# Kernel tuning notes

Hardware: AMD Instinct MI355X
Metric: run time of the kernel (lower is better)

## Reference

```python
import jax, jax.numpy as jnp
import numpy as np

B, N, D, H, DH, E, BIAS_DIM = 8, 512, 512, 8, 64, 32768, 8

def setup_inputs() -> dict:
    key = jax.random.key(0)
    ks = jax.random.split(key, 10)
    states = jax.random.normal(ks[0], (B, N, D), jnp.float32)
    key_states = jax.random.normal(ks[1], (B, N, D), jnp.float32)
    # causal mask, broadcastable over heads: [B,1,N,N]
    masks = jnp.broadcast_to(jnp.tril(jnp.ones((N, N), jnp.float32)), (B, 1, N, N))
    edge_type = jax.random.randint(ks[2], (E, 1), 0, BIAS_DIM, jnp.int32)
    b_idx = jax.random.randint(ks[3], (E, 1), 0, B, jnp.int32)
    q_idx = jax.random.randint(ks[4], (E, 1), 0, N, jnp.int32)
    k_idx = jax.random.randint(ks[5], (E, 1), 0, N, jnp.int32)
    attention_bias = jnp.concatenate([edge_type, b_idx, q_idx, k_idx], axis=1)
    s = 0.05
    Wq = jax.random.normal(ks[6], (D, H, DH), jnp.float32) * s
    Wk = jax.random.normal(ks[7], (D, H, DH), jnp.float32) * s
    Wv = jax.random.normal(ks[8], (D, H, DH), jnp.float32) * s
    k2 = jax.random.split(ks[9], 3)
    Wo = jax.random.normal(k2[0], (H, DH, D), jnp.float32) * s
    bias_embs = jax.random.normal(k2[1], (BIAS_DIM, DH), jnp.float32) * s
    bias_scalar = jax.random.normal(k2[2], (DH, 1), jnp.float32) * s
    return {"states": states, "key_states": key_states, "masks": masks,
            "attention_bias": attention_bias, "Wq": Wq, "Wk": Wk, "Wv": Wv,
            "Wo": Wo, "bias_embs": bias_embs, "bias_scalar": bias_scalar}

def reference(states, key_states, masks, attention_bias, Wq, Wk, Wv, Wo, bias_embs, bias_scalar):
    q = jnp.einsum('btd,dha->btha', states, Wq)
    k = jnp.einsum('btd,dha->btha', key_states, Wk)
    v = jnp.einsum('btd,dha->btha', key_states, Wv)
    alpha = jnp.einsum('bkha,bqha->bhqk', k, q)  # [B,H,Q,K]
    # sparse edge bias: embed edge types, project to scalar, scatter into [B,Q,K]
    et = attention_bias[:, 0]
    bias_vals = (bias_embs[et] @ bias_scalar)[:, 0]  # [E]
    bq, bk = alpha.shape[2], alpha.shape[3]
    bias_mat = jnp.zeros((alpha.shape[0], bq, bk), alpha.dtype)
    bias_mat = bias_mat.at[attention_bias[:, 1], attention_bias[:, 2], attention_bias[:, 3]].add(bias_vals)
    summed_keys = jnp.sum(k, axis=-1)  # [B,K,H]
    alpha = alpha + jnp.einsum('bqk,bkh->bhqk', bias_mat, summed_keys)
    alpha = alpha * jax.lax.rsqrt(jnp.float32(DH))
    neg = jnp.finfo(jnp.float32).min
    alpha = alpha * masks + (1.0 - jnp.ceil(masks)) * neg
    alpha = jax.nn.softmax(alpha, axis=-1)
    alpha = alpha * masks
    context = jnp.einsum('bhqk,bkha->bqha', alpha, v)
    return jnp.einsum('btha,had->btd', context, Wo)
```

## Files before the change

### kernel.cpp

```cpp
#include <hip/hip_runtime.h>

typedef unsigned short u16;
typedef unsigned int u32;
typedef __bf16 bf16x8 __attribute__((ext_vector_type(8)));
typedef float f32x4 __attribute__((ext_vector_type(4)));
typedef u16 u16x8 __attribute__((ext_vector_type(8)));
typedef u16 u16x4 __attribute__((ext_vector_type(4)));


__device__ __forceinline__ u16 f2b(float f) {
  union { float f; u32 i; } v; v.f = f;
  u32 r = v.i + 0x7fffu + ((v.i >> 16) & 1u);
  return (u16)(r >> 16);
}
__device__ __forceinline__ float b2f(u16 u) {
  union { u32 i; float f; } v; v.i = ((u32)u) << 16; return v.f;
}

__global__ __launch_bounds__(256) void prologue(
    const float* __restrict__ states, const float* __restrict__ key_states,
    const float* __restrict__ Wq, const float* __restrict__ Wk,
    const float* __restrict__ Wv, const float* __restrict__ Wo,
    const int* __restrict__ ab, const float* __restrict__ be,
    const float* __restrict__ bsc,
    u16* __restrict__ sb, u16* __restrict__ kbin, u16* __restrict__ wbase,
    float* __restrict__ bias_mat, int n_edges) {
  __shared__ u16 t[32][33];
  __shared__ float tv[8];
  int bid = blockIdx.x;
  int tid = threadIdx.x;
  if (bid < 2048) {
    const float* src = (bid >= 1024) ? key_states : states;
    u16* dst = (bid >= 1024) ? kbin : sb;
    int gid = (bid & 1023) * 256 + tid;
    const float4* sp = (const float4*)src + (size_t)gid * 2;
    float4 x0 = sp[0], x1 = sp[1];
    u16x8 p;
    p[0] = f2b(x0.x); p[1] = f2b(x0.y); p[2] = f2b(x0.z); p[3] = f2b(x0.w);
    p[4] = f2b(x1.x); p[5] = f2b(x1.y); p[6] = f2b(x1.z); p[7] = f2b(x1.w);
    *(u16x8*)(dst + (size_t)gid * 8) = p;
  } else if (bid < 3072) {
    int tt = bid - 2048;
    int z = tt >> 8, rem = tt & 255;
    int bx = rem & 15, by = rem >> 4;
    const float* src; float sc = 1.f;
    if (z == 0)      { src = Wq; sc = 0.125f; }
    else if (z == 1) { src = Wk; }
    else if (z == 2) { src = Wv; }
    else             { src = Wo; }
    u16* dst = wbase + (size_t)z * 262144;
    int tx = tid & 31, ty = tid >> 5;
    int c0 = bx * 32, r0 = by * 32;
    #pragma unroll
    for (int i = ty; i < 32; i += 8) t[i][tx] = f2b(src[(r0 + i) * 512 + c0 + tx] * sc);
    __syncthreads();
    #pragma unroll
    for (int i = ty; i < 32; i += 8) dst[(c0 + i) * 512 + r0 + tx] = t[tx][i];
  } else {
    if (tid < 8) {
      float s = 0.f;
      #pragma unroll
      for (int a = 0; a < 64; a++) s += be[tid * 64 + a] * bsc[a];
      tv[tid] = s * 0.125f;
    }
    __syncthreads();
    int e = (bid - 3072) * 256 + tid;
    if (e < n_edges) {
      int et = ab[e * 4 + 0];
      int b  = ab[e * 4 + 1];
      int qi = ab[e * 4 + 2];
      int ki = ab[e * 4 + 3];
      atomicAdd(&bias_mat[((size_t)b * 512 + qi) * 512 + ki], tv[et]);
    }
  }
}

__global__ __launch_bounds__(256) void qkv_gemm(const u16* __restrict__ sb,
                                                const u16* __restrict__ kbin,
                                                const u16* __restrict__ wT,
                                                u16* __restrict__ qb,
                                                u16* __restrict__ kbo,
                                                u16* __restrict__ vtb,
                                                float* __restrict__ summed) {
  __shared__ u16 As[64 * 72];
  __shared__ u16 Bs[128 * 72];
  __shared__ float ssum[4][64];
  int tid = threadIdx.x;
  int lane = tid & 63, wave = tid >> 6;
  int quad = lane >> 4, ln = lane & 15;
  int row0 = blockIdx.x * 64;
  int col0 = blockIdx.y * 128;
  const u16* A = (col0 < 512) ? sb : kbin;
  int ara = tid >> 2, aca = (tid & 3) * 16;
  int arb = tid >> 1, acb = (tid & 1) * 32;

  f32x4 acc[4][2];
  #pragma unroll
  for (int i = 0; i < 4; i++)
    #pragma unroll
    for (int j = 0; j < 2; j++) acc[i][j] = (f32x4){0.f, 0.f, 0.f, 0.f};

  const u16* ap = A + (size_t)(row0 + ara) * 512 + aca;
  const u16* bp = wT + (size_t)(col0 + arb) * 512 + acb;

  u16x8 ra0, ra1, rb0, rb1, rb2, rb3;
  ra0 = *(const u16x8*)(ap + 0);  ra1 = *(const u16x8*)(ap + 8);
  rb0 = *(const u16x8*)(bp + 0);  rb1 = *(const u16x8*)(bp + 8);
  rb2 = *(const u16x8*)(bp + 16); rb3 = *(const u16x8*)(bp + 24);

  for (int k0 = 0; k0 < 512; k0 += 64) {
    __syncthreads();
    *(u16x8*)&As[ara * 72 + aca + 0] = ra0;  *(u16x8*)&As[ara * 72 + aca + 8] = ra1;
    *(u16x8*)&Bs[arb * 72 + acb + 0]  = rb0;  *(u16x8*)&Bs[arb * 72 + acb + 8]  = rb1;
    *(u16x8*)&Bs[arb * 72 + acb + 16] = rb2;  *(u16x8*)&Bs[arb * 72 + acb + 24] = rb3;
    __syncthreads();
    if (k0 < 448) {
      int kn = k0 + 64;
      ra0 = *(const u16x8*)(ap + kn + 0);  ra1 = *(const u16x8*)(ap + kn + 8);
      rb0 = *(const u16x8*)(bp + kn + 0);  rb1 = *(const u16x8*)(bp + kn + 8);
      rb2 = *(const u16x8*)(bp + kn + 16); rb3 = *(const u16x8*)(bp + kn + 24);
    }
    #pragma unroll
    for (int s = 0; s < 2; s++) {
      bf16x8 af[4], bfv[2];
      #pragma unroll
      for (int i = 0; i < 4; i++)
        af[i] = *(bf16x8*)&As[(i * 16 + ln) * 72 + s * 32 + quad * 8];
      #pragma unroll
      for (int j = 0; j < 2; j++)
        bfv[j] = *(bf16x8*)&Bs[(wave * 32 + j * 16 + ln) * 72 + s * 32 + quad * 8];
      #pragma unroll
      for (int i = 0; i < 4; i++)
        #pragma unroll
        for (int j = 0; j < 2; j++)
          acc[i][j] = __builtin_amdgcn_mfma_f32_16x16x32_bf16(af[i], bfv[j], acc[i][j], 0, 0, 0);
    }
  }

  int region = col0 >> 9;
  int nbase = col0 & 511;
  if (region <= 1) {
    u16* Cout = region ? kbo : qb;
    #pragma unroll
    for (int i = 0; i < 4; i++)
      #pragma unroll
      for (int j = 0; j < 2; j++) {
        int mb = row0 + i * 16 + quad * 4;
        int n = nbase + wave * 32 + j * 16 + ln;
        #pragma unroll
        for (int r = 0; r < 4; r++)
          Cout[(size_t)(mb + r) * 512 + n] = f2b(acc[i][j][r]);
      }
    if (region == 1) {
      #pragma unroll
      for (int i = 0; i < 4; i++)
        #pragma unroll
        for (int r = 0; r < 4; r++) {
          float v = acc[i][0][r] + acc[i][1][r];
          v += __shfl_xor(v, 1);
          v += __shfl_xor(v, 2);
          v += __shfl_xor(v, 4);
          v += __shfl_xor(v, 8);
          if (ln == 0) ssum[wave][i * 16 + quad * 4 + r] = v;
        }
      __syncthreads();
      if (tid < 128) {
        int hl = tid >> 6, row = tid & 63;
        float s = ssum[hl * 2][row] + ssum[hl * 2 + 1][row];
        int m = row0 + row;
        int b = m >> 9, t = m & 511;
        int h = (nbase >> 6) + hl;
        summed[((size_t)(b * 8 + h)) * 512 + t] = s;
      }
    }
  } else {
    #pragma unroll
    for (int i = 0; i < 4; i++)
      #pragma unroll
      for (int j = 0; j < 2; j++) {
        int mb = row0 + i * 16 + quad * 4;
        int bb = mb >> 9, t0 = mb & 511;
        int a_abs = nbase + wave * 32 + j * 16 + ln;
        int h = a_abs >> 6, a = a_abs & 63;
        u16x4 p;
        p[0] = f2b(acc[i][j][0]); p[1] = f2b(acc[i][j][1]);
        p[2] = f2b(acc[i][j][2]); p[3] = f2b(acc[i][j][3]);
        *(u16x4*)&vtb[(((size_t)bb * 8 + h) * 64 + a) * 512 + t0] = p;
      }
  }
}

__global__ __launch_bounds__(256) void out_gemm(const u16* __restrict__ A,
                                                const u16* __restrict__ BT,
                                                float* __restrict__ C) {
  __shared__ u16 As[64 * 72];
  __shared__ u16 Bs[64 * 72];
  int tid = threadIdx.x;
  int lane = tid & 63, wave = tid >> 6;
  int quad = lane >> 4, ln = lane & 15;
  int wr = wave >> 1, wc = wave & 1;
  int row0 = blockIdx.x * 64;
  int col0 = blockIdx.y * 64;
  int ar = tid >> 2, ac = (tid & 3) * 16;

  f32x4 acc[2][2];
  #pragma unroll
  for (int i = 0; i < 2; i++)
    #pragma unroll
    for (int j = 0; j < 2; j++) acc[i][j] = (f32x4){0.f, 0.f, 0.f, 0.f};

  const u16* ap = A + (size_t)(row0 + ar) * 512 + ac;
  const u16* bp = BT + (size_t)(col0 + ar) * 512 + ac;

  u16x8 ra0, ra1, rb0, rb1;
  ra0 = *(const u16x8*)(ap + 0); ra1 = *(const u16x8*)(ap + 8);
  rb0 = *(const u16x8*)(bp + 0); rb1 = *(const u16x8*)(bp + 8);

  for (int k0 = 0; k0 < 512; k0 += 64) {
    __syncthreads();
    *(u16x8*)&As[ar * 72 + ac + 0] = ra0;  *(u16x8*)&As[ar * 72 + ac + 8] = ra1;
    *(u16x8*)&Bs[ar * 72 + ac + 0] = rb0;  *(u16x8*)&Bs[ar * 72 + ac + 8] = rb1;
    __syncthreads();
    if (k0 < 448) {
      int kn = k0 + 64;
      ra0 = *(const u16x8*)(ap + kn + 0); ra1 = *(const u16x8*)(ap + kn + 8);
      rb0 = *(const u16x8*)(bp + kn + 0); rb1 = *(const u16x8*)(bp + kn + 8);
    }
    #pragma unroll
    for (int s = 0; s < 2; s++) {
      bf16x8 af[2], bfv[2];
      #pragma unroll
      for (int i = 0; i < 2; i++)
        af[i] = *(bf16x8*)&As[(wr * 32 + i * 16 + ln) * 72 + s * 32 + quad * 8];
      #pragma unroll
      for (int j = 0; j < 2; j++)
        bfv[j] = *(bf16x8*)&Bs[(wc * 32 + j * 16 + ln) * 72 + s * 32 + quad * 8];
      #pragma unroll
      for (int i = 0; i < 2; i++)
        #pragma unroll
        for (int j = 0; j < 2; j++)
          acc[i][j] = __builtin_amdgcn_mfma_f32_16x16x32_bf16(af[i], bfv[j], acc[i][j], 0, 0, 0);
    }
  }
  #pragma unroll
  for (int i = 0; i < 2; i++)
    #pragma unroll
    for (int j = 0; j < 2; j++) {
      int mb = row0 + wr * 32 + i * 16 + quad * 4;
      int n = col0 + wc * 32 + j * 16 + ln;
      #pragma unroll
      for (int r = 0; r < 4; r++)
        C[(size_t)(mb + r) * 512 + n] = acc[i][j][r];
    }
}

__global__ __launch_bounds__(256) void attn_mfma(const u16* __restrict__ q,
                                                 const u16* __restrict__ k,
                                                 const u16* __restrict__ vt,
                                                 const float* __restrict__ bias_mat,
                                                 const float* __restrict__ summed,
                                                 u16* __restrict__ ctx,
                                                 float* __restrict__ Opart,
                                                 float* __restrict__ ml) {
  __shared__ u16 Qs[64 * 72];
  __shared__ u16 Ks[64 * 72];
  __shared__ u16 Vt[64 * 72];
  __shared__ u16 Ps[4][16 * 72];
  int tid = threadIdx.x;
  int wave = tid >> 6, lane = tid & 63;
  int quad = lane >> 4, ln = lane & 15;
  int p2 = blockIdx.x;
  int bh, u;
  {
    const int fours[6] = {3, 4, 6, 8, 10, 11};
    const int threes[2] = {2, 9};
    const int ones[2] = {0, 5};
    const int twos[2] = {1, 7};
    if (p2 < 384)      { bh = p2 & 63; u = fours[p2 >> 6]; }
    else if (p2 < 512) { int q2 = p2 - 384; bh = q2 & 63; u = threes[q2 >> 6]; }
    else if (p2 < 640) { int q2 = p2 - 512; bh = q2 & 63; u = ones[q2 >> 6]; }
    else               { int q2 = p2 - 640; bh = q2 & 63; u = twos[q2 >> 6]; }
  }
  int b = bh >> 3, h = bh & 7;
  int qt, kb0, kbe, part = 0;
  bool partial;
  if (u < 4) { qt = u; kb0 = 0; kbe = u; partial = false; }
  else {
    int v = u - 4; qt = 4 + (v >> 1); part = v & 1; partial = true;
    if (part == 0) { kb0 = 0; kbe = 3; } else { kb0 = 4; kbe = qt; }
  }
  int q0 = qt * 64;

  int sr = tid >> 2;
  int sc2 = (tid & 3) * 16;

  {
    const u16* qp = q + ((size_t)(b * 512 + q0 + sr)) * 512 + h * 64 + sc2;
    *(u16x8*)&Qs[sr * 72 + sc2] = *(const u16x8*)qp;
    *(u16x8*)&Qs[sr * 72 + sc2 + 8] = *(const u16x8*)(qp + 8);
  }

  float m_r[4], l_r[4];
  f32x4 o[4];
  #pragma unroll
  for (int r = 0; r < 4; r++) { m_r[r] = -3.40282347e38f; l_r[r] = 0.f; }
  #pragma unroll
  for (int nt = 0; nt < 4; nt++) o[nt] = (f32x4){0.f, 0.f, 0.f, 0.f};

  const u16* kp0 = k + ((size_t)(b * 512 + sr)) * 512 + h * 64 + sc2;
  const u16* vp0 = vt + ((size_t)(bh * 64 + sr)) * 512 + sc2;

  u16x8 rk0 = *(const u16x8*)(kp0 + (size_t)kb0 * 64 * 512);
  u16x8 rk1 = *(const u16x8*)(kp0 + (size_t)kb0 * 64 * 512 + 8);
  u16x8 rv0 = *(const u16x8*)(vp0 + kb0 * 64);
  u16x8 rv1 = *(const u16x8*)(vp0 + kb0 * 64 + 8);

  int qrow = q0 + wave * 16 + quad * 4;

  float c_skv[4], c_bias[4][4];
  #pragma unroll
  for (int nt = 0; nt < 4; nt++) {
    int t = kb0 * 64 + nt * 16 + ln;
    c_skv[nt] = summed[bh * 512 + t];
    const float* bp2 = bias_mat + ((size_t)(b * 512 + qrow)) * 512 + t;
    #pragma unroll
    for (int r = 0; r < 4; r++) c_bias[nt][r] = bp2[(size_t)r * 512];
  }

  for (int kb = kb0; kb <= kbe; kb++) {
    __syncthreads();
    *(u16x8*)&Ks[sr * 72 + sc2] = rk0;
    *(u16x8*)&Ks[sr * 72 + sc2 + 8] = rk1;
    *(u16x8*)&Vt[sr * 72 + sc2] = rv0;
    *(u16x8*)&Vt[sr * 72 + sc2 + 8] = rv1;
    __syncthreads();

    float n_skv[4], n_bias[4][4];
    if (kb < kbe) {
      const u16* kp = kp0 + (size_t)(kb + 1) * 64 * 512;
      const u16* vp = vp0 + (kb + 1) * 64;
      rk0 = *(const u16x8*)kp;
      rk1 = *(const u16x8*)(kp + 8);
      rv0 = *(const u16x8*)vp;
      rv1 = *(const u16x8*)(vp + 8);
      #pragma unroll
      for (int nt = 0; nt < 4; nt++) {
        int t = (kb + 1) * 64 + nt * 16 + ln;
        n_skv[nt] = summed[bh * 512 + t];
        const float* bp2 = bias_mat + ((size_t)(b * 512 + qrow)) * 512 + t;
        #pragma unroll
        for (int r = 0; r < 4; r++) n_bias[nt][r] = bp2[(size_t)r * 512];
      }
    }

    bf16x8 aq0 = *(bf16x8*)&Qs[(wave * 16 + ln) * 72 + quad * 8];
    bf16x8 aq1 = *(bf16x8*)&Qs[(wave * 16 + ln) * 72 + 32 + quad * 8];
    f32x4 s[4];
    #pragma unroll
    for (int nt = 0; nt < 4; nt++) {
      bf16x8 b0 = *(bf16x8*)&Ks[(nt * 16 + ln) * 72 + quad * 8];
      bf16x8 b1 = *(bf16x8*)&Ks[(nt * 16 + ln) * 72 + 32 + quad * 8];
      s[nt] = (f32x4){0.f, 0.f, 0.f, 0.f};
      s[nt] = __builtin_amdgcn_mfma_f32_16x16x32_bf16(aq0, b0, s[nt], 0, 0, 0);
      s[nt] = __builtin_amdgcn_mfma_f32_16x16x32_bf16(aq1, b1, s[nt], 0, 0, 0);
    }

    #pragma unroll
    for (int nt = 0; nt < 4; nt++) {
      int t = kb * 64 + nt * 16 + ln;
      #pragma unroll
      for (int r = 0; r < 4; r++) {
        float val = s[nt][r] + c_bias[nt][r] * c_skv[nt];
        s[nt][r] = (t <= qrow + r) ? val : -3.40282347e38f;
      }
    }

    float alpha[4];
    #pragma unroll
    for (int r = 0; r < 4; r++) {
      float tm = fmaxf(fmaxf(s[0][r], s[1][r]), fmaxf(s[2][r], s[3][r]));
      #pragma unroll
      for (int off = 8; off; off >>= 1) tm = fmaxf(tm, __shfl_xor(tm, off));
      float mn = fmaxf(m_r[r], tm);
      alpha[r] = __expf(m_r[r] - mn);
      m_r[r] = mn;
      float rs = 0.f;
      #pragma unroll
      for (int nt = 0; nt < 4; nt++) {
        float pp = __expf(s[nt][r] - mn);
        s[nt][r] = pp;
        rs += pp;
      }
      #pragma unroll
      for (int off = 8; off; off >>= 1) rs += __shfl_xor(rs, off);
      l_r[r] = l_r[r] * alpha[r] + rs;
    }

    #pragma unroll
    for (int nt = 0; nt < 4; nt++)
      #pragma unroll
      for (int r = 0; r < 4; r++)
        Ps[wave][(quad * 4 + r) * 72 + nt * 16 + ln] = f2b(s[nt][r]);
    #pragma unroll
    for (int nt = 0; nt < 4; nt++)
      #pragma unroll
      for (int r = 0; r < 4; r++)
        o[nt][r] *= alpha[r];

    bf16x8 ap0 = *(bf16x8*)&Ps[wave][ln * 72 + quad * 8];
    bf16x8 ap1 = *(bf16x8*)&Ps[wave][ln * 72 + 32 + quad * 8];
    #pragma unroll
    for (int nt = 0; nt < 4; nt++) {
      bf16x8 b0 = *(bf16x8*)&Vt[(nt * 16 + ln) * 72 + quad * 8];
      bf16x8 b1 = *(bf16x8*)&Vt[(nt * 16 + ln) * 72 + 32 + quad * 8];
      o[nt] = __builtin_amdgcn_mfma_f32_16x16x32_bf16(ap0, b0, o[nt], 0, 0, 0);
      o[nt] = __builtin_amdgcn_mfma_f32_16x16x32_bf16(ap1, b1, o[nt], 0, 0, 0);
    }

    if (kb < kbe) {
      #pragma unroll
      for (int nt = 0; nt < 4; nt++) {
        c_skv[nt] = n_skv[nt];
        #pragma unroll
        for (int r = 0; r < 4; r++) c_bias[nt][r] = n_bias[nt][r];
      }
    }
  }

  if (!partial) {
    #pragma unroll
    for (int r = 0; r < 4; r++) {
      float inv = 1.f / l_r[r];
      int qr2 = qrow + r;
      u16* dst = ctx + ((size_t)(b * 512 + qr2)) * 512 + h * 64;
      #pragma unroll
      for (int nt = 0; nt < 4; nt++)
        dst[nt * 16 + ln] = f2b(o[nt][r] * inv);
    }
  } else {
    #pragma unroll
    for (int r = 0; r < 4; r++) {
      int row = qrow + r - 256;
      float* dst = Opart + (((size_t)(part * 64 + bh)) * 256 + row) * 64;
      #pragma unroll
      for (int nt = 0; nt < 4; nt++)
        dst[nt * 16 + ln] = o[nt][r];
    }
    if (ln == 0) {
      #pragma unroll
      for (int r = 0; r < 4; r++) {
        int row = qrow + r - 256;
        float* mp = ml + (((size_t)(part * 64 + bh)) * 256 + row) * 2;
        mp[0] = m_r[r];
        mp[1] = l_r[r];
      }
    }
  }
}

__global__ __launch_bounds__(256) void attn_merge(const float* __restrict__ Opart,
                                                  const float* __restrict__ ml,
                                                  u16* __restrict__ ctx) {
  int gid = blockIdx.x * 256 + threadIdx.x;
  int col = gid & 63;
  int row = (gid >> 6) & 255;
  int bh = gid >> 14;
  size_t i0 = (size_t)bh * 256 + row;
  size_t i1 = (size_t)(64 + bh) * 256 + row;
  float m0 = ml[i0 * 2], l0 = ml[i0 * 2 + 1];
  float m1 = ml[i1 * 2], l1 = ml[i1 * 2 + 1];
  float m = fmaxf(m0, m1);
  float a0 = __expf(m0 - m), a1 = __expf(m1 - m);
  float l = l0 * a0 + l1 * a1;
  float O0 = Opart[i0 * 64 + col], O1 = Opart[i1 * 64 + col];
  float val = (O0 * a0 + O1 * a1) / l;
  int b = bh >> 3, h = bh & 7, qrow = 256 + row;
  ctx[((size_t)(b * 512 + qrow)) * 512 + h * 64 + col] = f2b(val);
}

extern "C" void kernel_launch(void* const* d_in, const int* in_sizes, int n_in,
                              void* d_out, int out_size, void* d_ws, size_t ws_size,
                              hipStream_t stream) {
  const float* states     = (const float*)d_in[0];
  const float* key_states = (const float*)d_in[1];
  const int*   ab         = (const int*)d_in[3];
  const float* Wq         = (const float*)d_in[4];
  const float* Wk         = (const float*)d_in[5];
  const float* Wv         = (const float*)d_in[6];
  const float* Wo         = (const float*)d_in[7];
  const float* be         = (const float*)d_in[8];
  const float* bsc        = (const float*)d_in[9];
  float* out = (float*)d_out;

  char* ws = (char*)d_ws;
  const size_t MB = 1024 * 1024;
  u16* wbase    = (u16*)(ws);
  u16* wot      = (u16*)(ws + 1536 * 1024);
  u16* sb       = (u16*)(ws + 2 * MB);
  u16* kbin     = (u16*)(ws + 6 * MB);
  u16* qb       = (u16*)(ws + 10 * MB);
  u16* kbo      = (u16*)(ws + 14 * MB);
  u16* vtb      = (u16*)(ws + 18 * MB);
  u16* ctxb     = (u16*)(ws + 22 * MB);
  float* bias_m = (float*)(ws + 26 * MB);
  float* summed = (float*)(ws + 34 * MB);
  float* Opart  = (float*)(ws + 35 * MB);
  float* mlbuf  = (float*)(ws + 43 * MB);

  int n_edges = in_sizes[3] / 4;

  hipMemsetAsync(bias_m, 0, (size_t)8 * MB, stream);
  prologue<<<dim3(3072 + (n_edges + 255) / 256), 256, 0, stream>>>(
      states, key_states, Wq, Wk, Wv, Wo, ab, be, bsc, sb, kbin, wbase, bias_m, n_edges);
  qkv_gemm<<<dim3(64, 12), 256, 0, stream>>>(sb, kbin, wbase, qb, kbo, vtb, summed);
  attn_mfma<<<dim3(768), 256, 0, stream>>>(qb, kbo, vtb, bias_m, summed, ctxb, Opart, mlbuf);
  attn_merge<<<dim3(4096), 256, 0, stream>>>(Opart, mlbuf, ctxb);
  out_gemm<<<dim3(64, 8), 256, 0, stream>>>(ctxb, wot, out);
}
```

Measured before the change: 133.9 us.

## Stage GEMM and attention tiles via direct global-to-LDS loads with double buffering

Replaces the register-staged global-to-shared copies in the QKV GEMM, the output GEMM and the attention kernel with global_load_lds 16-byte transfers. These write straight into double-buffered, XOR-swizzled shared-memory tiles, and the swizzle replaces the old row padding to avoid bank conflicts. Each k-step now needs only one barrier instead of two, and the next tile's load overlaps the current tile's MFMA work. In exchange, shared memory roughly doubles for the K/V and GEMM tiles, which may lower occupancy. Correctness also depends on the async LDS writes having completed before the barrier.

```diff
diff --git a/kernel.cpp b/kernel.cpp
--- a/kernel.cpp
+++ b/kernel.cpp
@@ -15,6 +15,33 @@
 }
 __device__ __forceinline__ float b2f(u16 u) {
   union { u32 i; float f; } v; v.i = ((u32)u) << 16; return v.f;
+}
+
+#define GLL16(gp, lp)                                                      \
+  __builtin_amdgcn_global_load_lds(                                       \
+      (const __attribute__((address_space(1))) u32*)(gp),                 \
+      (__attribute__((address_space(3))) u32*)(lp), 16, 0, 0)
+
+__device__ __forceinline__ void stage64(const u16* g, u16* l, int wave, int lane) {
+  int rsub = lane >> 3;
+  int gs = (((lane & 7) ^ rsub) << 3);
+  #pragma unroll
+  for (int c = 0; c < 2; c++) {
+    int ch = wave * 2 + c;
+    GLL16(g + (size_t)(ch * 8 + rsub) * 512 + gs, l + ch * 512);
+  }
+}
+__device__ __forceinline__ void stage128(const u16* g, u16* l, int wave, int lane) {
+  int rsub = lane >> 3;
+  int gs = (((lane & 7) ^ rsub) << 3);
+  #pragma unroll
+  for (int c = 0; c < 4; c++) {
+    int ch = wave * 4 + c;
+    GLL16(g + (size_t)(ch * 8 + rsub) * 512 + gs, l + ch * 512);
+  }
+}
+__device__ __forceinline__ int swz(int row, int g) {
+  return row * 64 + ((g ^ (row & 7)) << 3);
 }
 
 __global__ __launch_bounds__(256) void prologue(
@@ -82,8 +109,8 @@
                                                 u16* __restrict__ kbo,
                                                 u16* __restrict__ vtb,
                                                 float* __restrict__ summed) {
-  __shared__ u16 As[64 * 72];
-  __shared__ u16 Bs[128 * 72];
+  __shared__ alignas(16) u16 As[2][64 * 64];
+  __shared__ alignas(16) u16 Bs[2][128 * 64];
   __shared__ float ssum[4][64];
   int tid = threadIdx.x;
   int lane = tid & 63, wave = tid >> 6;
@@ -91,8 +118,8 @@
   int row0 = blockIdx.x * 64;
   int col0 = blockIdx.y * 128;
   const u16* A = (col0 < 512) ? sb : kbin;
-  int ara = tid >> 2, aca = (tid & 3) * 16;
-  int arb = tid >> 1, acb = (tid & 1) * 32;
+  const u16* Ab = A + (size_t)row0 * 512;
+  const u16* Bb = wT + (size_t)col0 * 512;
 
   f32x4 acc[4][2];
   #pragma unroll
@@ -100,41 +127,32 @@
     #pragma unroll
     for (int j = 0; j < 2; j++) acc[i][j] = (f32x4){0.f, 0.f, 0.f, 0.f};
 
-  const u16* ap = A + (size_t)(row0 + ara) * 512 + aca;
-  const u16* bp = wT + (size_t)(col0 + arb) * 512 + acb;
-
-  u16x8 ra0, ra1, rb0, rb1, rb2, rb3;
-  ra0 = *(const u16x8*)(ap + 0);  ra1 = *(const u16x8*)(ap + 8);
-  rb0 = *(const u16x8*)(bp + 0);  rb1 = *(const u16x8*)(bp + 8);
-  rb2 = *(const u16x8*)(bp + 16); rb3 = *(const u16x8*)(bp + 24);
-
+  stage64(Ab, As[0], wave, lane);
+  stage128(Bb, Bs[0], wave, lane);
+
+  int cur = 0;
   for (int k0 = 0; k0 < 512; k0 += 64) {
     __syncthreads();
-    *(u16x8*)&As[ara * 72 + aca + 0] = ra0;  *(u16x8*)&As[ara * 72 + aca + 8] = ra1;
-    *(u16x8*)&Bs[arb * 72 + acb + 0]  = rb0;  *(u16x8*)&Bs[arb * 72 + acb + 8]  = rb1;
-    *(u16x8*)&Bs[arb * 72 + acb + 16] = rb2;  *(u16x8*)&Bs[arb * 72 + acb + 24] = rb3;
-    __syncthreads();
     if (k0 < 448) {
-      int kn = k0 + 64;
-      ra0 = *(const u16x8*)(ap + kn + 0);  ra1 = *(const u16x8*)(ap + kn + 8);
-      rb0 = *(const u16x8*)(bp + kn + 0);  rb1 = *(const u16x8*)(bp + kn + 8);
-      rb2 = *(const u16x8*)(bp + kn + 16); rb3 = *(const u16x8*)(bp + kn + 24);
+      stage64(Ab + k0 + 64, As[cur ^ 1], wave, lane);
+      stage128(Bb + k0 + 64, Bs[cur ^ 1], wave, lane);
     }
     #pragma unroll
     for (int s = 0; s < 2; s++) {
       bf16x8 af[4], bfv[2];
       #pragma unroll
       for (int i = 0; i < 4; i++)
-        af[i] = *(bf16x8*)&As[(i * 16 + ln) * 72 + s * 32 + quad * 8];
+        af[i] = *(bf16x8*)&As[cur][swz(i * 16 + ln, s * 4 + quad)];
       #pragma unroll
       for (int j = 0; j < 2; j++)
-        bfv[j] = *(bf16x8*)&Bs[(wave * 32 + j * 16 + ln) * 72 + s * 32 + quad * 8];
+        bfv[j] = *(bf16x8*)&Bs[cur][swz(wave * 32 + j * 16 + ln, s * 4 + quad)];
       #pragma unroll
       for (int i = 0; i < 4; i++)
         #pragma unroll
         for (int j = 0; j < 2; j++)
           acc[i][j] = __builtin_amdgcn_mfma_f32_16x16x32_bf16(af[i], bfv[j], acc[i][j], 0, 0, 0);
     }
+    cur ^= 1;
   }
 
   int region = col0 >> 9;
@@ -193,15 +211,16 @@
 __global__ __launch_bounds__(256) void out_gemm(const u16* __restrict__ A,
                                                 const u16* __restrict__ BT,
                                                 float* __restrict__ C) {
-  __shared__ u16 As[64 * 72];
-  __shared__ u16 Bs[64 * 72];
+  __shared__ alignas(16) u16 As[2][64 * 64];
+  __shared__ alignas(16) u16 Bs[2][64 * 64];
   int tid = threadIdx.x;
   int lane = tid & 63, wave = tid >> 6;
   int quad = lane >> 4, ln = lane & 15;
   int wr = wave >> 1, wc = wave & 1;
   int row0 = blockIdx.x * 64;
   int col0 = blockIdx.y * 64;
-  int ar = tid >> 2, ac = (tid & 3) * 16;
+  const u16* Ab = A + (size_t)row0 * 512;
+  const u16* Bb = BT + (size_t)col0 * 512;
 
   f32x4 acc[2][2];
   #pragma unroll
@@ -209,38 +228,32 @@
     #pragma unroll
     for (int j = 0; j < 2; j++) acc[i][j] = (f32x4){0.f, 0.f, 0.f, 0.f};
 
-  const u16* ap = A + (size_t)(row0 + ar) * 512 + ac;
-  const u16* bp = BT + (size_t)(col0 + ar) * 512 + ac;
-
-  u16x8 ra0, ra1, rb0, rb1;
-  ra0 = *(const u16x8*)(ap + 0); ra1 = *(const u16x8*)(ap + 8);
-  rb0 = *(const u16x8*)(bp + 0); rb1 = *(const u16x8*)(bp + 8);
-
+  stage64(Ab, As[0], wave, lane);
+  stage64(Bb, Bs[0], wave, lane);
+
+  int cur = 0;
   for (int k0 = 0; k0 < 512; k0 += 64) {
     __syncthreads();
-    *(u16x8*)&As[ar * 72 + ac + 0] = ra0;  *(u16x8*)&As[ar * 72 + ac + 8] = ra1;
-    *(u16x8*)&Bs[ar * 72 + ac + 0] = rb0;  *(u16x8*)&Bs[ar * 72 + ac + 8] = rb1;
-    __syncthreads();
     if (k0 < 448) {
-      int kn = k0 + 64;
-      ra0 = *(const u16x8*)(ap + kn + 0); ra1 = *(const u16x8*)(ap + kn + 8);
-      rb0 = *(const u16x8*)(bp + kn + 0); rb1 = *(const u16x8*)(bp + kn + 8);
+      stage64(Ab + k0 + 64, As[cur ^ 1], wave, lane);
+      stage64(Bb + k0 + 64, Bs[cur ^ 1], wave, lane);
     }
     #pragma unroll
     for (int s = 0; s < 2; s++) {
       bf16x8 af[2], bfv[2];
       #pragma unroll
       for (int i = 0; i < 2; i++)
-        af[i] = *(bf16x8*)&As[(wr * 32 + i * 16 + ln) * 72 + s * 32 + quad * 8];
+        af[i] = *(bf16x8*)&As[cur][swz(wr * 32 + i * 16 + ln, s * 4 + quad)];
       #pragma unroll
       for (int j = 0; j < 2; j++)
-        bfv[j] = *(bf16x8*)&Bs[(wc * 32 + j * 16 + ln) * 72 + s * 32 + quad * 8];
+        bfv[j] = *(bf16x8*)&Bs[cur][swz(wc * 32 + j * 16 + ln, s * 4 + quad)];
       #pragma unroll
       for (int i = 0; i < 2; i++)
         #pragma unroll
         for (int j = 0; j < 2; j++)
           acc[i][j] = __builtin_amdgcn_mfma_f32_16x16x32_bf16(af[i], bfv[j], acc[i][j], 0, 0, 0);
     }
+    cur ^= 1;
   }
   #pragma unroll
   for (int i = 0; i < 2; i++)
@@ -262,10 +275,10 @@
                                                  u16* __restrict__ ctx,
                                                  float* __restrict__ Opart,
                                                  float* __restrict__ ml) {
-  __shared__ u16 Qs[64 * 72];
-  __shared__ u16 Ks[64 * 72];
-  __shared__ u16 Vt[64 * 72];
-  __shared__ u16 Ps[4][16 * 72];
+  __shared__ alignas(16) u16 Qs[64 * 64];
+  __shared__ alignas(16) u16 Ks[2][64 * 64];
+  __shared__ alignas(16) u16 Vs[2][64 * 64];
+  __shared__ alignas(16) u16 Ps[4][16 * 72];
   int tid = threadIdx.x;
   int wave = tid >> 6, lane = tid & 63;
   int quad = lane >> 4, ln = lane & 15;
@@ -291,14 +304,13 @@
   }
   int q0 = qt * 64;
 
-  int sr = tid >> 2;
-  int sc2 = (tid & 3) * 16;
-
-  {
-    const u16* qp = q + ((size_t)(b * 512 + q0 + sr)) * 512 + h * 64 + sc2;
-    *(u16x8*)&Qs[sr * 72 + sc2] = *(const u16x8*)qp;
-    *(u16x8*)&Qs[sr * 72 + sc2 + 8] = *(const u16x8*)(qp + 8);
-  }
+  const u16* qb_ = q + ((size_t)(b * 512 + q0)) * 512 + h * 64;
+  const u16* kb_ = k + ((size_t)(b * 512)) * 512 + h * 64;
+  const u16* vb_ = vt + ((size_t)bh * 64) * 512;
+
+  stage64(qb_, Qs, wave, lane);
+  stage64(kb_ + (size_t)kb0 * 64 * 512, Ks[0], wave, lane);
+  stage64(vb_ + kb0 * 64, Vs[0], wave, lane);
 
   float m_r[4], l_r[4];
   f32x4 o[4];
@@ -306,14 +318,6 @@
   for (int r = 0; r < 4; r++) { m_r[r] = -3.40282347e38f; l_r[r] = 0.f; }
   #pragma unroll
   for (int nt = 0; nt < 4; nt++) o[nt] = (f32x4){0.f, 0.f, 0.f, 0.f};
-
-  const u16* kp0 = k + ((size_t)(b * 512 + sr)) * 512 + h * 64 + sc2;
-  const u16* vp0 = vt + ((size_t)(bh * 64 + sr)) * 512 + sc2;
-
-  u16x8 rk0 = *(const u16x8*)(kp0 + (size_t)kb0 * 64 * 512);
-  u16x8 rk1 = *(const u16x8*)(kp0 + (size_t)kb0 * 64 * 512 + 8);
-  u16x8 rv0 = *(const u16x8*)(vp0 + kb0 * 64);
-  u16x8 rv1 = *(const u16x8*)(vp0 + kb0 * 64 + 8);
 
   int qrow = q0 + wave * 16 + quad * 4;
 
@@ -327,22 +331,14 @@
     for (int r = 0; r < 4; r++) c_bias[nt][r] = bp2[(size_t)r * 512];
   }
 
+  int cur = 0;
   for (int kb = kb0; kb <= kbe; kb++) {
     __syncthreads();
-    *(u16x8*)&Ks[sr * 72 + sc2] = rk0;
-    *(u16x8*)&Ks[sr * 72 + sc2 + 8] = rk1;
-    *(u16x8*)&Vt[sr * 72 + sc2] = rv0;
-    *(u16x8*)&Vt[sr * 72 + sc2 + 8] = rv1;
-    __syncthreads();
 
     float n_skv[4], n_bias[4][4];
     if (kb < kbe) {
-      const u16* kp = kp0 + (size_t)(kb + 1) * 64 * 512;
-      const u16* vp = vp0 + (kb + 1) * 64;
-      rk0 = *(const u16x8*)kp;
-      rk1 = *(const u16x8*)(kp + 8);
-      rv0 = *(const u16x8*)vp;
-      rv1 = *(const u16x8*)(vp + 8);
+      stage64(kb_ + (size_t)(kb + 1) * 64 * 512, Ks[cur ^ 1], wave, lane);
+      stage64(vb_ + (kb + 1) * 64, Vs[cur ^ 1], wave, lane);
       #pragma unroll
       for (int nt = 0; nt < 4; nt++) {
         int t = (kb + 1) * 64 + nt * 16 + ln;
@@ -353,13 +349,13 @@
       }
     }
 
-    bf16x8 aq0 = *(bf16x8*)&Qs[(wave * 16 + ln) * 72 + quad * 8];
-    bf16x8 aq1 = *(bf16x8*)&Qs[(wave * 16 + ln) * 72 + 32 + quad * 8];
+    bf16x8 aq0 = *(bf16x8*)&Qs[swz(wave * 16 + ln, quad)];
+    bf16x8 aq1 = *(bf16x8*)&Qs[swz(wave * 16 + ln, 4 + quad)];
     f32x4 s[4];
     #pragma unroll
     for (int nt = 0; nt < 4; nt++) {
-      bf16x8 b0 = *(bf16x8*)&Ks[(nt * 16 + ln) * 72 + quad * 8];
-      bf16x8 b1 = *(bf16x8*)&Ks[(nt * 16 + ln) * 72 + 32 + quad * 8];
+      bf16x8 b0 = *(bf16x8*)&Ks[cur][swz(nt * 16 + ln, quad)];
+      bf16x8 b1 = *(bf16x8*)&Ks[cur][swz(nt * 16 + ln, 4 + quad)];
       s[nt] = (f32x4){0.f, 0.f, 0.f, 0.f};
       s[nt] = __builtin_amdgcn_mfma_f32_16x16x32_bf16(aq0, b0, s[nt], 0, 0, 0);
       s[nt] = __builtin_amdgcn_mfma_f32_16x16x32_bf16(aq1, b1, s[nt], 0, 0, 0);
@@ -411,8 +407,8 @@
     bf16x8 ap1 = *(bf16x8*)&Ps[wave][ln * 72 + 32 + quad * 8];
     #pragma unroll
     for (int nt = 0; nt < 4; nt++) {
-      bf16x8 b0 = *(bf16x8*)&Vt[(nt * 16 + ln) * 72 + quad * 8];
-      bf16x8 b1 = *(bf16x8*)&Vt[(nt * 16 + ln) * 72 + 32 + quad * 8];
+      bf16x8 b0 = *(bf16x8*)&Vs[cur][swz(nt * 16 + ln, quad)];
+      bf16x8 b1 = *(bf16x8*)&Vs[cur][swz(nt * 16 + ln, 4 + quad)];
       o[nt] = __builtin_amdgcn_mfma_f32_16x16x32_bf16(ap0, b0, o[nt], 0, 0, 0);
       o[nt] = __builtin_amdgcn_mfma_f32_16x16x32_bf16(ap1, b1, o[nt], 0, 0, 0);
     }
@@ -425,6 +421,7 @@
         for (int r = 0; r < 4; r++) c_bias[nt][r] = n_bias[nt][r];
       }
     }
+    cur ^= 1;
   }
 
   if (!partial) {
```

Measured after the change: 134.6 us. No clear change (+0.6%).
